# Kernel optimization log

Hardware: AMD Instinct MI355X
Metric: run time of the kernel (lower is better)

The kernel has to match this reference:

```python
import jax, jax.numpy as jnp
import numpy as np
from jax import lax

T_SIZE = 8        # frames
S_SIZE = 14       # spatial grid side
N_HEAD = 16
D_MODEL = 1024
L = S_SIZE * S_SIZE          # 196 patch tokens per frame
N_BATCH = 8


def _layernorm(x, g, b):
    # torch LayerNorm subclass computes in fp32 then casts back
    x32 = x.astype(jnp.float32)
    m = x32.mean(-1, keepdims=True)
    v = x32.var(-1, keepdims=True)
    return ((x32 - m) * lax.rsqrt(v + 1e-5) * g + b).astype(x.dtype)


def _mha(x, wqkv, bqkv, wo, bo, bias):
    # x: [S, B, C] seq-first like torch MHA; bias: [n_head, S, S] or None
    S, B, C = x.shape
    hd = C // N_HEAD
    qkv = x @ wqkv.T + bqkv
    q, k, v = jnp.split(qkv, 3, axis=-1)
    def h(t):
        return t.reshape(S, B, N_HEAD, hd).transpose(1, 2, 0, 3)  # [B,H,S,hd]
    q = h(q) * (1.0 / np.sqrt(hd))
    k, v = h(k), h(v)
    scores = jnp.einsum('bhqd,bhkd->bhqk', q, k)
    if bias is not None:
        scores = scores + bias[None]  # broadcast over batch (torch repeats; same math)
    a = jax.nn.softmax(scores, axis=-1)
    o = jnp.einsum('bhqk,bhkd->bhqd', a, v).transpose(2, 0, 1, 3).reshape(S, B, C)
    return o @ wo.T + bo


def _rel_idx():
    t = jnp.arange(T_SIZE)
    idx_t = t[:, None] - t[None, :] + T_SIZE - 1          # [T,T]
    c = jnp.arange(L)
    qi, qj = c // S_SIZE, c % S_SIZE
    i_off = qi[:, None] - qi[None, :] + S_SIZE - 1
    j_off = qj[:, None] - qj[None, :] + S_SIZE - 1
    idx_s = i_off * (2 * S_SIZE - 1) + j_off              # [L,L]
    return idx_t, idx_s


def reference(x, pos_w, pos_b, ln_t_g, ln_t_b, rpb_t, wqkv_t, bqkv_t, wo_t, bo_t,
              ln1_g, ln1_b, rpb_s, wqkv_s, bqkv_s, wo_s, bo_s,
              ln2_g, ln2_b, fc_w, fc_b, proj_w, proj_b):
    T, S, H, C = T_SIZE, S_SIZE, N_HEAD, D_MODEL
    LT = L * T
    N = x.shape[1]
    idx_t, idx_s = _rel_idx()

    # depthwise 3D conv positional embedding on patch tokens (token order is (h w t))
    v = x[1:].reshape(S, S, T, N, C).transpose(3, 4, 2, 0, 1)  # [N,C,T,H,W]
    conv = lax.conv_general_dilated(
        v, pos_w, (1, 1, 1), [(1, 1), (1, 1), (1, 1)],
        dimension_numbers=('NCDHW', 'OIDHW', 'NCDHW'),
        feature_group_count=C) + pos_b[None, :, None, None, None]
    tmp = (v + conv).reshape(N, C, T, L).transpose(3, 2, 0, 1).reshape(LT, N, C)
    x = jnp.concatenate([x[:1], tmp], 0)

    # temporal attention: '(l t) n c -> t (n l) c'
    xt = x[1:].reshape(L, T, N, C).transpose(1, 2, 0, 3).reshape(T, N * L, C)
    bias_t = rpb_t[idx_t].transpose(2, 0, 1)  # [H,T,T]
    rt = _mha(_layernorm(xt, ln_t_g, ln_t_b), wqkv_t, bqkv_t, wo_t, bo_t, bias_t)
    rt = rt.reshape(T, N, L, C).transpose(2, 0, 1, 3).reshape(LT, N, C)
    xt_full = x[1:] + rt

    # spatial attention with replicated cls token: 'l (t n) c' batching
    cls = jnp.tile(x[:1], (1, T, 1))                      # [1, T*N, C], t-major
    xs = jnp.concatenate([cls, xt_full.reshape(L, T * N, C)], 0)  # [L+1, T*N, C]
    bias_s = jnp.zeros((H, L + 1, L + 1), x.dtype).at[:, 1:, 1:].set(
        rpb_s[idx_s].transpose(2, 0, 1))
    rs = _mha(_layernorm(xs, ln1_g, ln1_b), wqkv_s, bqkv_s, wo_s, bo_s, bias_s)
    cls_out = rs[0].reshape(T, N, C).mean(0, keepdims=True)       # mean over frames
    spa = rs[1:].reshape(LT, N, C)                                # 'l (t n) -> (l t) n'
    x = x + jnp.concatenate([cls_out, spa], 0)

    # MLP with QuickGELU
    h = _layernorm(x, ln2_g, ln2_b) @ fc_w.T + fc_b
    h = h * jax.nn.sigmoid(1.702 * h)
    return x + (h @ proj_w.T + proj_b)


def setup_inputs() -> dict:
    key = jax.random.key(0)
    ks = jax.random.split(key, 12)
    C = D_MODEL
    f32 = jnp.float32
    def w(k, shape, s=0.02):
        return jax.random.normal(k, shape, f32) * s
    return {
        'x': jax.random.normal(ks[0], (1 + L * T_SIZE, N_BATCH, C), f32),
        'pos_w': w(ks[1], (C, 1, 3, 3, 3)),
        'pos_b': jnp.zeros((C,), f32),
        'ln_t_g': jnp.ones((C,), f32), 'ln_t_b': jnp.zeros((C,), f32),
        'rpb_t': w(ks[2], (2 * T_SIZE - 1, N_HEAD)),
        'wqkv_t': w(ks[3], (3 * C, C)), 'bqkv_t': jnp.zeros((3 * C,), f32),
        'wo_t': w(ks[4], (C, C)), 'bo_t': jnp.zeros((C,), f32),
        'ln1_g': jnp.ones((C,), f32), 'ln1_b': jnp.zeros((C,), f32),
        'rpb_s': w(ks[5], ((2 * S_SIZE - 1) ** 2, N_HEAD)),
        'wqkv_s': w(ks[6], (3 * C, C)), 'bqkv_s': jnp.zeros((3 * C,), f32),
        'wo_s': w(ks[7], (C, C)), 'bo_s': jnp.zeros((C,), f32),
        'ln2_g': jnp.ones((C,), f32), 'ln2_b': jnp.zeros((C,), f32),
        'fc_w': w(ks[8], (4 * C, C)), 'fc_b': jnp.zeros((4 * C,), f32),
        'proj_w': w(ks[9], (C, 4 * C)), 'proj_b': jnp.zeros((C,), f32),
    }
```

## Files before the change

kernel.cpp:

```cpp
#include <hip/hip_runtime.h>
#include <stdint.h>

typedef unsigned short u16;
typedef __attribute__((ext_vector_type(8))) __bf16 bf16x8;
typedef __attribute__((ext_vector_type(4))) float f32x4;

__device__ __forceinline__ float bf2f(u16 u) {
    return __uint_as_float(((unsigned int)u) << 16);
}
__device__ __forceinline__ u16 f2bf(float f) {
    unsigned int u = __float_as_uint(f);
    u += 0x7fffu + ((u >> 16) & 1u);
    return (u16)(u >> 16);
}

__device__ __forceinline__ void gl16(const u16* g, u16* l) {
    __builtin_amdgcn_global_load_lds(
        (const __attribute__((address_space(1))) unsigned int*)(uintptr_t)g,
        (__attribute__((address_space(3))) unsigned int*)(uintptr_t)l,
        16, 0, 0);
}

__global__ __launch_bounds__(256) void cvt_bf16(const float4* __restrict__ in,
                                                ushort4* __restrict__ out, int n4) {
    int tid = blockIdx.x * 256 + threadIdx.x;
    if (tid < n4) {
        float4 v = in[tid];
        ushort4 o;
        o.x = f2bf(v.x); o.y = f2bf(v.y); o.z = f2bf(v.z); o.w = f2bf(v.w);
        out[tid] = o;
    }
}

__global__ __launch_bounds__(256) void cvt_wt(const float* __restrict__ pw,
                                              float* __restrict__ wt) {
    int tid = blockIdx.x * 256 + threadIdx.x;
    if (tid < 27648) {
        int tap = tid >> 10, c = tid & 1023;
        wt[tid] = pw[c * 27 + tap];
    }
}

__global__ __launch_bounds__(256) void posembed(const float4* __restrict__ x4,
                                                const float4* __restrict__ wt4,
                                                const float4* __restrict__ pb4,
                                                float4* __restrict__ out4) {
    int tid = blockIdx.x * 256 + threadIdx.x;
    float4 xv = x4[tid];
    int rf = tid >> 11;
    if (rf == 0) { out4[tid] = xv; return; }
    int c4 = tid & 255;
    int n = (tid >> 8) & 7;
    int r = rf - 1;
    int t = r & 7, l = r >> 3;
    int i = l / 14, j = l - i * 14;
    float4 pbv = pb4[c4];
    float a0 = xv.x + pbv.x, a1 = xv.y + pbv.y, a2 = xv.z + pbv.z, a3 = xv.w + pbv.w;
#pragma unroll
    for (int dt = 0; dt < 3; dt++) {
        int tt = t + dt - 1;
        if (tt < 0 || tt > 7) continue;
#pragma unroll
        for (int di = 0; di < 3; di++) {
            int ii = i + di - 1;
            if (ii < 0 || ii > 13) continue;
#pragma unroll
            for (int dj = 0; dj < 3; dj++) {
                int jj = j + dj - 1;
                if (jj < 0 || jj > 13) continue;
                float4 w4 = wt4[(dt * 9 + di * 3 + dj) * 256 + c4];
                float4 v = x4[(size_t)(1 + ((ii * 14 + jj) << 3) + tt) * 2048 + (n << 8) + c4];
                a0 += w4.x * v.x; a1 += w4.y * v.y; a2 += w4.z * v.z; a3 += w4.w * v.w;
            }
        }
    }
    out4[tid] = (float4){a0, a1, a2, a3};
}

__global__ __launch_bounds__(256) void ln_kernel(const float* __restrict__ resid,
                                                 const u16* __restrict__ Radd,
                                                 const float* __restrict__ g,
                                                 const float* __restrict__ bb,
                                                 u16* __restrict__ out, int mode) {
    int ro = blockIdx.x;
    int tid = threadIdx.x;
    int src, n;
    long long rarow = -1;
    if (mode == 0) {
        int t = ro / 1568, b2 = ro - t * 1568;
        n = b2 / 196;
        int l = b2 - n * 196;
        src = 1 + l * 8 + t;
    } else if (mode == 1) {
        int s = ro >> 6, u = ro & 63;
        int t = u >> 3;
        n = u & 7;
        if (s == 0) src = 0;
        else { src = 1 + (s - 1) * 8 + t; rarow = (long long)(t * 1568 + n * 196 + (s - 1)); }
    } else {
        src = ro >> 3;
        n = ro & 7;
    }
    const float* xp = resid + ((size_t)src * 8 + n) * 1024 + tid * 4;
    float4 xv = *(const float4*)xp;
    float x0 = xv.x, x1 = xv.y, x2 = xv.z, x3 = xv.w;
    if (rarow >= 0) {
        const u16* rp = Radd + rarow * 1024 + tid * 4;
        x0 += bf2f(rp[0]); x1 += bf2f(rp[1]); x2 += bf2f(rp[2]); x3 += bf2f(rp[3]);
    }
    float s1 = x0 + x1 + x2 + x3;
    float s2 = x0 * x0 + x1 * x1 + x2 * x2 + x3 * x3;
#pragma unroll
    for (int off = 32; off > 0; off >>= 1) {
        s1 += __shfl_down(s1, off);
        s2 += __shfl_down(s2, off);
    }
    __shared__ float red[8];
    int lane = tid & 63, w = tid >> 6;
    if (lane == 0) { red[w] = s1; red[4 + w] = s2; }
    __syncthreads();
    float S1 = red[0] + red[1] + red[2] + red[3];
    float S2 = red[4] + red[5] + red[6] + red[7];
    float mean = S1 * (1.f / 1024.f);
    float var = S2 * (1.f / 1024.f) - mean * mean;
    float rstd = rsqrtf(var + 1e-5f);
    int c = tid * 4;
    u16* op = out + (size_t)ro * 1024 + c;
    op[0] = f2bf((x0 - mean) * rstd * g[c + 0] + bb[c + 0]);
    op[1] = f2bf((x1 - mean) * rstd * g[c + 1] + bb[c + 1]);
    op[2] = f2bf((x2 - mean) * rstd * g[c + 2] + bb[c + 2]);
    op[3] = f2bf((x3 - mean) * rstd * g[c + 3] + bb[c + 3]);
}

__global__ __launch_bounds__(256) void gemm_bf16(const u16* __restrict__ A,
                                                 const u16* __restrict__ W,
                                                 const float* __restrict__ bias,
                                                 u16* __restrict__ Co,
                                                 int M, int N, int K, int gelu) {
    __shared__ u16 As[128 * 32];
    __shared__ u16 Bs[128 * 32];
    int tid = threadIdx.x;
    int n0 = blockIdx.x * 128, m0 = blockIdx.y * 128;
    int lane = tid & 63, wid = tid >> 6;
    int wm = (wid >> 1) * 64, wn = (wid & 1) * 64;
    int lm = lane & 15, q = lane >> 4;

    f32x4 acc[4][4];
#pragma unroll
    for (int i = 0; i < 4; i++)
#pragma unroll
        for (int j = 0; j < 4; j++) acc[i][j] = (f32x4){0.f, 0.f, 0.f, 0.f};

    int r0 = wid * 32 + (lane >> 2);
    int colb = (lane & 3) * 8;
    int mA0 = m0 + r0;          if (mA0 > M - 1) mA0 = M - 1;
    int mA1 = m0 + r0 + 16;     if (mA1 > M - 1) mA1 = M - 1;
    const u16* gA0 = A + (size_t)mA0 * K + colb;
    const u16* gA1 = A + (size_t)mA1 * K + colb;
    const u16* gB0 = W + (size_t)(n0 + r0) * K + colb;
    const u16* gB1 = W + (size_t)(n0 + r0 + 16) * K + colb;
    u16* lA0 = &As[wid * 1024];
    u16* lA1 = &As[wid * 1024 + 512];
    u16* lB0 = &Bs[wid * 1024];
    u16* lB1 = &Bs[wid * 1024 + 512];

    for (int k0 = 0; k0 < K; k0 += 32) {
        gl16(gA0, lA0); gl16(gA1, lA1);
        gl16(gB0, lB0); gl16(gB1, lB1);
        gA0 += 32; gA1 += 32; gB0 += 32; gB1 += 32;
        __syncthreads();
        bf16x8 af[4], bfr[4];
#pragma unroll
        for (int i = 0; i < 4; i++) af[i] = *(const bf16x8*)&As[(wm + i * 16 + lm) * 32 + q * 8];
#pragma unroll
        for (int j = 0; j < 4; j++) bfr[j] = *(const bf16x8*)&Bs[(wn + j * 16 + lm) * 32 + q * 8];
#pragma unroll
        for (int i = 0; i < 4; i++)
#pragma unroll
            for (int j = 0; j < 4; j++)
                acc[i][j] = __builtin_amdgcn_mfma_f32_16x16x32_bf16(af[i], bfr[j], acc[i][j], 0, 0, 0);
        __syncthreads();
    }

#pragma unroll
    for (int i = 0; i < 4; i++) {
        int row_b = m0 + wm + i * 16 + q * 4;
#pragma unroll
        for (int j = 0; j < 4; j++) {
            int col = n0 + wn + j * 16 + lm;
            float bv = bias[col];
#pragma unroll
            for (int r = 0; r < 4; r++) {
                int row = row_b + r;
                if (row < M) {
                    float v = acc[i][j][r] + bv;
                    if (gelu) v = v / (1.f + __expf(-1.702f * v));
                    Co[(size_t)row * N + col] = f2bf(v);
                }
            }
        }
    }
}

__global__ __launch_bounds__(64) void attn_t(const u16* __restrict__ qkv,
                                             const float* __restrict__ rpb,
                                             u16* __restrict__ out) {
    int blk = blockIdx.x;
    int b = blk % 1568, h = blk / 1568;
    int d = threadIdx.x;
    __shared__ float qs[8][65], ks[8][65], vs[8][65];
    __shared__ float ps[8][9];
#pragma unroll
    for (int t = 0; t < 8; t++) {
        size_t row = (size_t)(t * 1568 + b) * 3072 + h * 64 + d;
        qs[t][d] = bf2f(qkv[row]) * 0.125f;
        ks[t][d] = bf2f(qkv[row + 1024]);
        vs[t][d] = bf2f(qkv[row + 2048]);
    }
    __syncthreads();
    int tq = d >> 3, tk = d & 7;
    float s = rpb[(tq - tk + 7) * 16 + h];
#pragma unroll
    for (int dd = 0; dd < 64; dd++) s += qs[tq][dd] * ks[tk][dd];
    float mx = s;
    mx = fmaxf(mx, __shfl_xor(mx, 1));
    mx = fmaxf(mx, __shfl_xor(mx, 2));
    mx = fmaxf(mx, __shfl_xor(mx, 4));
    float p = __expf(s - mx);
    float su = p;
    su += __shfl_xor(su, 1);
    su += __shfl_xor(su, 2);
    su += __shfl_xor(su, 4);
    ps[tq][tk] = p / su;
    __syncthreads();
#pragma unroll
    for (int t2 = 0; t2 < 8; t2++) {
        float o = 0.f;
#pragma unroll
        for (int k2 = 0; k2 < 8; k2++) o += ps[t2][k2] * vs[k2][d];
        out[(size_t)(t2 * 1568 + b) * 1024 + h * 64 + d] = f2bf(o);
    }
}

#define KLS 72
#define PVS 232
__global__ __launch_bounds__(256) void attn_s(const u16* __restrict__ qkv,
                                              const float* __restrict__ rpb,
                                              u16* __restrict__ out) {
    __shared__ u16 Kl[208 * KLS];
    __shared__ u16 Vt[64 * PVS];
    __shared__ u16 Pl[4][16 * PVS];
    __shared__ float rpb_l[736];
    int blk = blockIdx.x;
    int u = blk & 63, h = blk >> 6;
    int tid = threadIdx.x;
    int w = tid >> 6, lane = tid & 63;
    int lm = lane & 15, quad = lane >> 4;

    for (int idx = tid; idx < 197 * 8; idx += 256) {
        int s = idx >> 3, c8 = idx & 7;
        const u16* gp = qkv + (size_t)(s * 64 + u) * 3072 + h * 64 + c8 * 8;
        uint4 kv = *(const uint4*)(gp + 1024);
        uint4 vv = *(const uint4*)(gp + 2048);
        *(uint4*)&Kl[s * KLS + c8 * 8] = kv;
        const u16* vp = (const u16*)&vv;
#pragma unroll
        for (int j = 0; j < 8; j++) Vt[(c8 * 8 + j) * PVS + s] = vp[j];
    }
    for (int i = tid; i < 11 * KLS; i += 256) Kl[197 * KLS + i] = 0;
    for (int i = tid; i < 64 * 35; i += 256) {
        int dd = i / 35, c = 197 + (i - dd * 35);
        Vt[dd * PVS + c] = 0;
    }
    {
        for (int i = lane; i < 256; i += 64) {
            int r = i >> 4, c = 208 + (i & 15);
            Pl[w][r * PVS + c] = 0;
        }
    }
    for (int i = tid; i < 729; i += 256) rpb_l[i] = rpb[i * 16 + h];
    __syncthreads();

    for (int it = 0; it < 4; it++) {
        int qt = it * 4 + w;
        bool act = qt < 13;
        f32x4 sc[13];
        float rs[4];
        if (act) {
            int qrow = qt * 16 + lm;
            int srq = qrow > 196 ? 196 : qrow;
            const u16* qp = qkv + (size_t)(srq * 64 + u) * 3072 + h * 64 + quad * 8;
            bf16x8 aq0 = *(const bf16x8*)qp;
            bf16x8 aq1 = *(const bf16x8*)(qp + 32);
            for (int kt = 0; kt < 13; kt++) {
                bf16x8 bk0 = *(const bf16x8*)&Kl[(kt * 16 + lm) * KLS + quad * 8];
                bf16x8 bk1 = *(const bf16x8*)&Kl[(kt * 16 + lm) * KLS + 32 + quad * 8];
                f32x4 s = __builtin_amdgcn_mfma_f32_16x16x32_bf16(aq0, bk0, (f32x4){0.f, 0.f, 0.f, 0.f}, 0, 0, 0);
                sc[kt] = __builtin_amdgcn_mfma_f32_16x16x32_bf16(aq1, bk1, s, 0, 0, 0);
            }
            int tk = lm;
#pragma unroll
            for (int r = 0; r < 4; r++) {
                int qr = qt * 16 + quad * 4 + r;
                int qcl = qr > 196 ? 196 : qr;
                int lq = qcl - 1;
                int qi = lq / 14, qj = lq - qi * 14;
                for (int kt = 0; kt < 13; kt++) {
                    int tkk = kt * 16 + tk;
                    float v;
                    if (tkk >= 197) v = -1e30f;
                    else {
                        v = sc[kt][r] * 0.125f;
                        if (qr >= 1 && tkk >= 1) {
                            int lk = tkk - 1;
                            int ki = lk / 14, kj = lk - ki * 14;
                            v += rpb_l[(qi - ki + 13) * 27 + (qj - kj + 13)];
                        }
                    }
                    sc[kt][r] = v;
                }
                float mx = -3e38f;
                for (int kt = 0; kt < 13; kt++) mx = fmaxf(mx, sc[kt][r]);
                mx = fmaxf(mx, __shfl_xor(mx, 1));
                mx = fmaxf(mx, __shfl_xor(mx, 2));
                mx = fmaxf(mx, __shfl_xor(mx, 4));
                mx = fmaxf(mx, __shfl_xor(mx, 8));
                float sm = 0.f;
                for (int kt = 0; kt < 13; kt++) {
                    float p = __expf(sc[kt][r] - mx);
                    sc[kt][r] = p;
                    sm += p;
                }
                sm += __shfl_xor(sm, 1);
                sm += __shfl_xor(sm, 2);
                sm += __shfl_xor(sm, 4);
                sm += __shfl_xor(sm, 8);
                rs[r] = sm;
                for (int kt = 0; kt < 13; kt++)
                    Pl[w][(quad * 4 + r) * PVS + kt * 16 + tk] = f2bf(sc[kt][r]);
            }
        }
        __syncthreads();
        if (act) {
            bf16x8 pa[7];
#pragma unroll
            for (int kc = 0; kc < 7; kc++)
                pa[kc] = *(const bf16x8*)&Pl[w][lm * PVS + kc * 32 + quad * 8];
#pragma unroll
            for (int ct = 0; ct < 4; ct++) {
                f32x4 o = (f32x4){0.f, 0.f, 0.f, 0.f};
#pragma unroll
                for (int kc = 0; kc < 7; kc++) {
                    bf16x8 vb = *(const bf16x8*)&Vt[(ct * 16 + lm) * PVS + kc * 32 + quad * 8];
                    o = __builtin_amdgcn_mfma_f32_16x16x32_bf16(pa[kc], vb, o, 0, 0, 0);
                }
#pragma unroll
                for (int r = 0; r < 4; r++) {
                    int qr = qt * 16 + quad * 4 + r;
                    if (qr < 197)
                        out[(size_t)(qr * 64 + u) * 1024 + h * 64 + ct * 16 + lm] =
                            f2bf(o[r] / rs[r]);
                }
            }
        }
        __syncthreads();
    }
}

__global__ __launch_bounds__(256) void add_cls(const u16* __restrict__ R, float4* __restrict__ resid4) {
    int tid = blockIdx.x * 256 + threadIdx.x;
    int c4 = tid & 255, n = tid >> 8;
    float s0 = 0.f, s1 = 0.f, s2 = 0.f, s3 = 0.f;
#pragma unroll
    for (int t = 0; t < 8; t++) {
        ushort4 rv = *(const ushort4*)&R[(size_t)(t * 8 + n) * 1024 + c4 * 4];
        s0 += bf2f(rv.x); s1 += bf2f(rv.y); s2 += bf2f(rv.z); s3 += bf2f(rv.w);
    }
    float4 v = resid4[tid];
    v.x += s0 * 0.125f; v.y += s1 * 0.125f; v.z += s2 * 0.125f; v.w += s3 * 0.125f;
    resid4[tid] = v;
}

__global__ __launch_bounds__(256) void add_spa(const u16* __restrict__ R, float4* __restrict__ resid4) {
    int tid = blockIdx.x * 256 + threadIdx.x;
    int c4 = tid & 255;
    int n = (tid >> 8) & 7;
    int r = tid >> 11;
    int t = r & 7, l = r >> 3;
    int srow = (l + 1) * 64 + t * 8 + n;
    ushort4 rv = *(const ushort4*)&R[(size_t)srow * 1024 + c4 * 4];
    float4 v = resid4[tid + 2048];
    v.x += bf2f(rv.x); v.y += bf2f(rv.y); v.z += bf2f(rv.z); v.w += bf2f(rv.w);
    resid4[tid + 2048] = v;
}

__global__ __launch_bounds__(256) void add_flat(const ushort4* __restrict__ R4, float4* __restrict__ resid4) {
    int tid = blockIdx.x * 256 + threadIdx.x;
    ushort4 rv = R4[tid];
    float4 v = resid4[tid];
    v.x += bf2f(rv.x); v.y += bf2f(rv.y); v.z += bf2f(rv.z); v.w += bf2f(rv.w);
    resid4[tid] = v;
}

extern "C" void kernel_launch(void* const* d_in, const int* in_sizes, int n_in,
                              void* d_out, int out_size, void* d_ws, size_t ws_size,
                              hipStream_t stream) {
    const float* x      = (const float*)d_in[0];
    const float* pos_w  = (const float*)d_in[1];
    const float* pos_b  = (const float*)d_in[2];
    const float* ln_t_g = (const float*)d_in[3];
    const float* ln_t_b = (const float*)d_in[4];
    const float* rpb_t  = (const float*)d_in[5];
    const float* wqkv_t = (const float*)d_in[6];
    const float* bqkv_t = (const float*)d_in[7];
    const float* wo_t   = (const float*)d_in[8];
    const float* bo_t   = (const float*)d_in[9];
    const float* ln1_g  = (const float*)d_in[10];
    const float* ln1_b  = (const float*)d_in[11];
    const float* rpb_s  = (const float*)d_in[12];
    const float* wqkv_s = (const float*)d_in[13];
    const float* bqkv_s = (const float*)d_in[14];
    const float* wo_s   = (const float*)d_in[15];
    const float* bo_s   = (const float*)d_in[16];
    const float* ln2_g  = (const float*)d_in[17];
    const float* ln2_b  = (const float*)d_in[18];
    const float* fc_w   = (const float*)d_in[19];
    const float* fc_b   = (const float*)d_in[20];
    const float* proj_w = (const float*)d_in[21];
    const float* proj_b = (const float*)d_in[22];
    float* resid = (float*)d_out;

    u16* Wq_t  = (u16*)d_ws;
    u16* Wo_t  = Wq_t + 3145728;
    u16* Wq_s  = Wo_t + 1048576;
    u16* Wo_s  = Wq_s + 3145728;
    u16* Wfc   = Wo_s + 1048576;
    u16* Wpj   = Wfc  + 4194304;
    u16* Albuf = Wpj  + 4194304;
    u16* QKV   = Albuf + 12910592;
    u16* Obuf  = QKV   + 38731776;
    u16* Rbuf  = Obuf  + 12910592;
    u16* Hbuf  = QKV;
    float* wt  = (float*)QKV;

    cvt_bf16<<<3072, 256, 0, stream>>>((const float4*)wqkv_t, (ushort4*)Wq_t, 786432);
    cvt_bf16<<<1024, 256, 0, stream>>>((const float4*)wo_t,   (ushort4*)Wo_t, 262144);
    cvt_bf16<<<3072, 256, 0, stream>>>((const float4*)wqkv_s, (ushort4*)Wq_s, 786432);
    cvt_bf16<<<1024, 256, 0, stream>>>((const float4*)wo_s,   (ushort4*)Wo_s, 262144);
    cvt_bf16<<<4096, 256, 0, stream>>>((const float4*)fc_w,   (ushort4*)Wfc,  1048576);
    cvt_bf16<<<4096, 256, 0, stream>>>((const float4*)proj_w, (ushort4*)Wpj,  1048576);
    cvt_wt<<<108, 256, 0, stream>>>(pos_w, wt);

    posembed<<<12552, 256, 0, stream>>>((const float4*)x, (const float4*)wt,
                                        (const float4*)pos_b, (float4*)resid);

    ln_kernel<<<12544, 256, 0, stream>>>(resid, nullptr, ln_t_g, ln_t_b, Albuf, 0);
    gemm_bf16<<<dim3(24, 98), 256, 0, stream>>>(Albuf, Wq_t, bqkv_t, QKV, 12544, 3072, 1024, 0);
    attn_t<<<25088, 64, 0, stream>>>(QKV, rpb_t, Obuf);
    gemm_bf16<<<dim3(8, 98), 256, 0, stream>>>(Obuf, Wo_t, bo_t, Rbuf, 12544, 1024, 1024, 0);

    ln_kernel<<<12608, 256, 0, stream>>>(resid, Rbuf, ln1_g, ln1_b, Albuf, 1);
    gemm_bf16<<<dim3(24, 99), 256, 0, stream>>>(Albuf, Wq_s, bqkv_s, QKV, 12608, 3072, 1024, 0);
    attn_s<<<1024, 256, 0, stream>>>(QKV, rpb_s, Obuf);
    gemm_bf16<<<dim3(8, 99), 256, 0, stream>>>(Obuf, Wo_s, bo_s, Rbuf, 12608, 1024, 1024, 0);
    add_cls<<<8, 256, 0, stream>>>(Rbuf, (float4*)resid);
    add_spa<<<12544, 256, 0, stream>>>(Rbuf, (float4*)resid);

    ln_kernel<<<12552, 256, 0, stream>>>(resid, nullptr, ln2_g, ln2_b, Albuf, 2);
    gemm_bf16<<<dim3(32, 99), 256, 0, stream>>>(Albuf, Wfc, fc_b, Hbuf, 12552, 4096, 1024, 1);
    gemm_bf16<<<dim3(8, 99), 256, 0, stream>>>(Hbuf, Wpj, proj_b, Rbuf, 12552, 1024, 4096, 0);
    add_flat<<<12552, 256, 0, stream>>>((const ushort4*)Rbuf, (float4*)resid);
}
```

Before: 1.302 ms.

## Double-buffer GEMM LDS tiles and remap blocks across XCDs

The bf16 GEMM now keeps two LDS buffers so the next K-tile's global-to-LDS load is issued while MFMAs run on the current tile, needing one barrier per step instead of two. A 1D grid with a remapping by blockIdx mod 8 gives each group of consecutive blocks on the same XCD neighbouring output tiles, meant to improve L2 reuse of A and W. This doubles shared memory per block, which may lower occupancy. The loop assumes K/32 is even, which holds for the K values used here.

```diff
diff --git a/kernel.cpp b/kernel.cpp
--- a/kernel.cpp
+++ b/kernel.cpp
@@ -136,11 +136,16 @@
                                                  const u16* __restrict__ W,
                                                  const float* __restrict__ bias,
                                                  u16* __restrict__ Co,
-                                                 int M, int N, int K, int gelu) {
-    __shared__ u16 As[128 * 32];
-    __shared__ u16 Bs[128 * 32];
+                                                 int M, int N, int K, int gelu,
+                                                 int nx) {
+    __shared__ u16 As[2][128 * 32];
+    __shared__ u16 Bs[2][128 * 32];
     int tid = threadIdx.x;
-    int n0 = blockIdx.x * 128, m0 = blockIdx.y * 128;
+    int T = gridDim.x;
+    int bid = blockIdx.x;
+    int w_ = (bid & 7) * (T >> 3) + (bid >> 3);
+    int n0 = (w_ % nx) * 128;
+    int m0 = (w_ / nx) * 128;
     int lane = tid & 63, wid = tid >> 6;
     int wm = (wid >> 1) * 64, wn = (wid & 1) * 64;
     int lm = lane & 15, q = lane >> 4;
@@ -159,28 +164,35 @@
     const u16* gA1 = A + (size_t)mA1 * K + colb;
     const u16* gB0 = W + (size_t)(n0 + r0) * K + colb;
     const u16* gB1 = W + (size_t)(n0 + r0 + 16) * K + colb;
-    u16* lA0 = &As[wid * 1024];
-    u16* lA1 = &As[wid * 1024 + 512];
-    u16* lB0 = &Bs[wid * 1024];
-    u16* lB1 = &Bs[wid * 1024 + 512];
-
-    for (int k0 = 0; k0 < K; k0 += 32) {
-        gl16(gA0, lA0); gl16(gA1, lA1);
-        gl16(gB0, lB0); gl16(gB1, lB1);
+    int wo = wid * 1024;
+
+    auto loadt = [&](int b) {
+        gl16(gA0, &As[b][wo]); gl16(gA1, &As[b][wo + 512]);
+        gl16(gB0, &Bs[b][wo]); gl16(gB1, &Bs[b][wo + 512]);
         gA0 += 32; gA1 += 32; gB0 += 32; gB1 += 32;
-        __syncthreads();
+    };
+    auto comput = [&](int b) {
         bf16x8 af[4], bfr[4];
 #pragma unroll
-        for (int i = 0; i < 4; i++) af[i] = *(const bf16x8*)&As[(wm + i * 16 + lm) * 32 + q * 8];
-#pragma unroll
-        for (int j = 0; j < 4; j++) bfr[j] = *(const bf16x8*)&Bs[(wn + j * 16 + lm) * 32 + q * 8];
+        for (int i = 0; i < 4; i++) af[i] = *(const bf16x8*)&As[b][(wm + i * 16 + lm) * 32 + q * 8];
+#pragma unroll
+        for (int j = 0; j < 4; j++) bfr[j] = *(const bf16x8*)&Bs[b][(wn + j * 16 + lm) * 32 + q * 8];
 #pragma unroll
         for (int i = 0; i < 4; i++)
 #pragma unroll
             for (int j = 0; j < 4; j++)
                 acc[i][j] = __builtin_amdgcn_mfma_f32_16x16x32_bf16(af[i], bfr[j], acc[i][j], 0, 0, 0);
-        __syncthreads();
-    }
+    };
+
+    int Tt = K >> 5;
+    loadt(0);
+    __syncthreads();
+    loadt(1); comput(0); __syncthreads();
+    for (int t = 2; t + 1 < Tt; t += 2) {
+        loadt(0); comput(1); __syncthreads();
+        loadt(1); comput(0); __syncthreads();
+    }
+    comput(1);
 
 #pragma unroll
     for (int i = 0; i < 4; i++) {
@@ -455,19 +467,19 @@
                                         (const float4*)pos_b, (float4*)resid);
 
     ln_kernel<<<12544, 256, 0, stream>>>(resid, nullptr, ln_t_g, ln_t_b, Albuf, 0);
-    gemm_bf16<<<dim3(24, 98), 256, 0, stream>>>(Albuf, Wq_t, bqkv_t, QKV, 12544, 3072, 1024, 0);
+    gemm_bf16<<<2352, 256, 0, stream>>>(Albuf, Wq_t, bqkv_t, QKV, 12544, 3072, 1024, 0, 24);
     attn_t<<<25088, 64, 0, stream>>>(QKV, rpb_t, Obuf);
-    gemm_bf16<<<dim3(8, 98), 256, 0, stream>>>(Obuf, Wo_t, bo_t, Rbuf, 12544, 1024, 1024, 0);
+    gemm_bf16<<<784, 256, 0, stream>>>(Obuf, Wo_t, bo_t, Rbuf, 12544, 1024, 1024, 0, 8);
 
     ln_kernel<<<12608, 256, 0, stream>>>(resid, Rbuf, ln1_g, ln1_b, Albuf, 1);
-    gemm_bf16<<<dim3(24, 99), 256, 0, stream>>>(Albuf, Wq_s, bqkv_s, QKV, 12608, 3072, 1024, 0);
+    gemm_bf16<<<2376, 256, 0, stream>>>(Albuf, Wq_s, bqkv_s, QKV, 12608, 3072, 1024, 0, 24);
     attn_s<<<1024, 256, 0, stream>>>(QKV, rpb_s, Obuf);
-    gemm_bf16<<<dim3(8, 99), 256, 0, stream>>>(Obuf, Wo_s, bo_s, Rbuf, 12608, 1024, 1024, 0);
+    gemm_bf16<<<792, 256, 0, stream>>>(Obuf, Wo_s, bo_s, Rbuf, 12608, 1024, 1024, 0, 8);
     add_cls<<<8, 256, 0, stream>>>(Rbuf, (float4*)resid);
     add_spa<<<12544, 256, 0, stream>>>(Rbuf, (float4*)resid);
 
     ln_kernel<<<12552, 256, 0, stream>>>(resid, nullptr, ln2_g, ln2_b, Albuf, 2);
-    gemm_bf16<<<dim3(32, 99), 256, 0, stream>>>(Albuf, Wfc, fc_b, Hbuf, 12552, 4096, 1024, 1);
-    gemm_bf16<<<dim3(8, 99), 256, 0, stream>>>(Hbuf, Wpj, proj_b, Rbuf, 12552, 1024, 4096, 0);
+    gemm_bf16<<<3168, 256, 0, stream>>>(Albuf, Wfc, fc_b, Hbuf, 12552, 4096, 1024, 1, 32);
+    gemm_bf16<<<792, 256, 0, stream>>>(Hbuf, Wpj, proj_b, Rbuf, 12552, 1024, 4096, 0, 8);
     add_flat<<<12552, 256, 0, stream>>>((const ushort4*)Rbuf, (float4*)resid);
 }
```

Result: faster. 1.176 ms (-9.6%).
